# Performance work log

Measured on AMD Instinct MI355X. Metric: run time of the kernel, lower is better.

The kernel has to match this reference:

```python
import jax, jax.numpy as jnp
import numpy as np

NUM_JOINT_LIST = [8, 10, 12, 14, 16, 18, 20, 22, 24, 9, 13, 17]
NUM_GLOBAL_LIST = [1, 0, 1, 1, 0, 1, 1, 1, 0, 1, 1, 1]
M = len(NUM_JOINT_LIST)
B, T, JMAX = 16, 128, 24
H, HEADS, L, RANK = 256, 8, 4, 8
DH = H // HEADS
LAYERSCALE = 1e-4


def setup_inputs():
    key = jax.random.key(0)
    ks = jax.random.split(key, 40)
    m_idx = jax.random.randint(ks[0], (B,), 0, M)
    nj = jnp.array(NUM_JOINT_LIST)[m_idx]
    valid = jnp.arange(JMAX)[None, :] < nj[:, None]  # (B, J) real joints of each morphology
    jtype = jax.random.randint(ks[1], (B, JMAX), 0, 3)  # 0 slide, 1 hinge, 2 global
    has_g = (jnp.array(NUM_GLOBAL_LIST) > 0)[m_idx][:, None]
    jtype = jnp.where((jtype == 2) & ~has_g, 0, jtype)
    tile = lambda m: jnp.broadcast_to(m[:, None, :], (B, T, JMAX))
    slide_mask = tile((jtype == 0) & valid)
    hinge_mask = tile((jtype == 1) & valid)
    global_mask = tile((jtype == 2) & valid)
    act_mask = tile(valid)
    morph_mask = (valid[:, :, None] & valid[:, None, :]) | jnp.eye(JMAX, dtype=bool)[None]
    act = jax.random.normal(ks[2], (B, T, JMAX, 1), dtype=jnp.float32)
    s = 0.02
    inp = dict(act=act, slide_mask=slide_mask, hinge_mask=hinge_mask,
               global_mask=global_mask, act_mask=act_mask, morph_mask=morph_mask,
               m_idx=m_idx)
    inp['Ws'] = s * jax.random.normal(ks[3], (1, H)); inp['bs'] = jnp.zeros((H,))
    inp['Wh'] = s * jax.random.normal(ks[4], (1, H)); inp['bh'] = jnp.zeros((H,))
    inp['Wg'] = s * jax.random.normal(ks[5], (M, H))
    inp['Wact'] = s * jax.random.normal(ks[6], (1, H))
    pos = jax.random.normal(ks[7], (M, JMAX, H))
    pos_valid = jnp.arange(JMAX)[None, :, None] < jnp.array(NUM_JOINT_LIST)[:, None, None]
    inp['pos'] = pos * pos_valid  # rows beyond num_joint stay zero, as in the torch loop
    inp['ln1_s'] = jnp.ones((L, H)); inp['ln1_b'] = jnp.zeros((L, H))
    inp['Wqkv'] = s * jax.random.normal(ks[8], (L, H, 3 * H)); inp['bqkv'] = jnp.zeros((L, 3 * H))
    inp['loraA'] = s * jax.random.normal(ks[9], (L, M, H, RANK))
    inp['loraB'] = s * jax.random.normal(ks[10], (L, M, RANK, 3 * H))
    inp['Wo'] = s * jax.random.normal(ks[11], (L, H, H)); inp['bo'] = jnp.zeros((L, H))
    inp['ln2_s'] = jnp.ones((L, H)); inp['ln2_b'] = jnp.zeros((L, H))
    inp['W1'] = s * jax.random.normal(ks[12], (L, H, 4 * H)); inp['b1'] = jnp.zeros((L, 4 * H))
    inp['W2'] = s * jax.random.normal(ks[13], (L, 4 * H, H)); inp['b2'] = jnp.zeros((L, H))
    inp['g1'] = LAYERSCALE * jnp.ones((L, H)); inp['g2'] = LAYERSCALE * jnp.ones((L, H))
    inp['lnf_s'] = jnp.ones((H,)); inp['lnf_b'] = jnp.zeros((H,))
    return inp


def _ln(z, sc, bi):
    mu = z.mean(-1, keepdims=True)
    v = ((z - mu) ** 2).mean(-1, keepdims=True)
    return (z - mu) * jax.lax.rsqrt(v + 1e-5) * sc + bi


def reference(act, slide_mask, hinge_mask, global_mask, act_mask, morph_mask, m_idx,
              Ws, bs, Wh, bh, Wg, Wact, pos,
              ln1_s, ln1_b, Wqkv, bqkv, loraA, loraB, Wo, bo,
              ln2_s, ln2_b, W1, b1, W2, b2, g1, g2, lnf_s, lnf_b):
    has_g = (jnp.array(NUM_GLOBAL_LIST) > 0)[m_idx]  # (B,)
    a1 = act[..., :1]  # slide_dim = hinge_dim = num_global = 1
    emb = jnp.where(slide_mask[..., None], a1 @ Ws + bs, jnp.zeros((), act.dtype))
    emb = jnp.where(hinge_mask[..., None], a1 @ Wh + bh, emb)
    emb_g = a1 * Wg[m_idx][:, None, None, :]  # per-sample morphology-routed projection
    emb = jnp.where((global_mask & has_g[:, None, None])[..., None], emb_g, emb)
    y = emb + act_mask[..., None].astype(emb.dtype) * Wact[0]
    y = y + pos[m_idx][:, None]  # (B, T, J, H)
    Bv, Tv, J, _ = y.shape
    N = Bv * Tv
    x = y.reshape(N, J, H)
    amask = jnp.broadcast_to(morph_mask[:, None], (Bv, Tv, J, J)).reshape(N, J, J)
    t_idx = jnp.repeat(m_idx, Tv)  # (N,)
    neg = jnp.finfo(x.dtype).min
    scale = 1.0 / np.sqrt(DH)

    def block(x, lp):
        l1s, l1b, wqkv, bq, lA, lB, wo, bo_, l2s, l2b, w1, b1_, w2, b2_, gg1, gg2 = lp
        h = _ln(x, l1s, l1b)
        qkv = h @ wqkv + bq
        # per-task LoRA on qkv, gathered by morphology index
        qkv = qkv + jnp.einsum('njr,nrk->njk', jnp.einsum('njd,ndr->njr', h, lA[t_idx]), lB[t_idx])
        q, k, v = jnp.split(qkv, 3, axis=-1)
        q = q.reshape(N, J, HEADS, DH).transpose(0, 2, 1, 3)
        k = k.reshape(N, J, HEADS, DH).transpose(0, 2, 1, 3)
        v = v.reshape(N, J, HEADS, DH).transpose(0, 2, 1, 3)
        scores = jnp.einsum('nhid,nhjd->nhij', q, k) * scale
        scores = jnp.where(amask[:, None], scores, neg)
        attn = jax.nn.softmax(scores, axis=-1)
        o = jnp.einsum('nhij,nhjd->nhid', attn, v).transpose(0, 2, 1, 3).reshape(N, J, H)
        x = x + gg1 * (o @ wo + bo_)
        h2 = _ln(x, l2s, l2b)
        x = x + gg2 * (jax.nn.gelu(h2 @ w1 + b1_) @ w2 + b2_)
        return x, None

    x, _ = jax.lax.scan(block, x, (ln1_s, ln1_b, Wqkv, bqkv, loraA, loraB, Wo, bo,
                                   ln2_s, ln2_b, W1, b1, W2, b2, g1, g2))
    x = _ln(x, lnf_s, lnf_b)
    return x.reshape(Bv, Tv, J, H)
```

## Files before the change

### kernel.cpp

```cpp
#include <hip/hip_runtime.h>
#include <cstdint>
#include <cstddef>

#define B_     16
#define T_     128
#define J_     24
#define H_     256
#define HEADS_ 8
#define DH_    32
#define L_     4
#define RANK_  8
#define M_     12
#define NTOK   (B_*T_)
#define ROWS   (NTOK*J_)
#define HAS_G_MASK 3821

typedef __attribute__((ext_vector_type(8))) short short8;
typedef __attribute__((ext_vector_type(4))) float f32x4;

__constant__ int cNJ[M_] = {8, 10, 12, 14, 16, 18, 20, 22, 24, 9, 13, 17};

__device__ __forceinline__ float bf2f(unsigned short u) {
    union { unsigned int i; float f; } c; c.i = ((unsigned int)u) << 16; return c.f;
}
__device__ __forceinline__ unsigned short f2bf(float f) {
    union { float f; unsigned int i; } c; c.f = f;
    unsigned int x = c.i;
    return (unsigned short)((x + 0x7fffu + ((x >> 16) & 1u)) >> 16);
}
__device__ __forceinline__ void gload16(const void* g, void* l) {
    __builtin_amdgcn_global_load_lds((const __attribute__((address_space(1))) void*)g,
                                     (__attribute__((address_space(3))) void*)l, 16, 0, 0);
}

__global__ void zero_flag(int* f) { *f = 0; }

__global__ __launch_bounds__(256) void detect_kernel(
    const unsigned char* __restrict__ sl, const unsigned char* __restrict__ hi,
    const unsigned char* __restrict__ gl, const int* __restrict__ m_idx,
    int* __restrict__ flag) {
    int rj = blockIdx.x * 256 + threadIdx.x;
    if (rj >= ROWS) return;
    int b = rj / (T_ * J_);
    int j = rj % J_;
    int valid = (j < cNJ[m_idx[b]]) ? 1 : 0;
    int cnt = (sl[rj] != 0) + (hi[rj] != 0) + (gl[rj] != 0);
    if (cnt != valid) atomicOr(flag, 1);
}

__global__ void wconv_t(const float* __restrict__ W, unsigned short* __restrict__ WT,
                        int K, int Nc, int total) {
    int i = blockIdx.x * 256 + threadIdx.x;
    if (i >= total) return;
    int kn = K * Nc;
    int l = i / kn;
    int r = i - l * kn;
    int k = r / Nc;
    int n = r - k * Nc;
    WT[(size_t)l * kn + (size_t)n * K + k] = f2bf(W[i]);
}

__global__ __launch_bounds__(256) void embed_kernel(
    const float* __restrict__ act, const void* __restrict__ slide,
    const void* __restrict__ hinge, const void* __restrict__ glob,
    const int* __restrict__ m_idx, const int* __restrict__ flag,
    const float* __restrict__ Ws, const float* __restrict__ bs,
    const float* __restrict__ Wh, const float* __restrict__ bh,
    const float* __restrict__ Wg, const float* __restrict__ Wact,
    const float* __restrict__ pos, float* __restrict__ X) {
    int rj = (blockIdx.x << 2) + (threadIdx.x >> 6);
    int lane = threadIdx.x & 63;
    int b = rj / (T_ * J_);
    int j = rj % J_;
    int m = m_idx[b];
    bool valid = j < cNJ[m];
    bool s, hh, gl;
    if (*flag) {
        s  = ((const int*)slide)[rj] != 0;
        hh = ((const int*)hinge)[rj] != 0;
        gl = ((const int*)glob)[rj]  != 0;
    } else {
        s  = ((const unsigned char*)slide)[rj] != 0;
        hh = ((const unsigned char*)hinge)[rj] != 0;
        gl = ((const unsigned char*)glob)[rj]  != 0;
    }
    float a1 = act[rj];
    int h0 = lane << 2;
    float e0 = 0.f, e1 = 0.f, e2 = 0.f, e3 = 0.f;
    if (s) {
        float4 w = *(const float4*)(Ws + h0); float4 bb = *(const float4*)(bs + h0);
        e0 = a1 * w.x + bb.x; e1 = a1 * w.y + bb.y; e2 = a1 * w.z + bb.z; e3 = a1 * w.w + bb.w;
    } else if (hh) {
        float4 w = *(const float4*)(Wh + h0); float4 bb = *(const float4*)(bh + h0);
        e0 = a1 * w.x + bb.x; e1 = a1 * w.y + bb.y; e2 = a1 * w.z + bb.z; e3 = a1 * w.w + bb.w;
    } else if (gl && ((HAS_G_MASK >> m) & 1)) {
        float4 w = *(const float4*)(Wg + m * H_ + h0);
        e0 = a1 * w.x; e1 = a1 * w.y; e2 = a1 * w.z; e3 = a1 * w.w;
    }
    if (valid) {
        float4 wa = *(const float4*)(Wact + h0);
        e0 += wa.x; e1 += wa.y; e2 += wa.z; e3 += wa.w;
    }
    float4 pv = *(const float4*)(pos + (size_t)(m * J_ + j) * H_ + h0);
    float4 out; out.x = e0 + pv.x; out.y = e1 + pv.y; out.z = e2 + pv.z; out.w = e3 + pv.w;
    *(float4*)(X + ((size_t)rj << 8) + h0) = out;
}

template<bool LORA>
__global__ __launch_bounds__(256) void ln_kernel(
    const float* __restrict__ X, const float* __restrict__ sc, const float* __restrict__ bi,
    const float* __restrict__ lA, const int* __restrict__ m_idx,
    unsigned short* __restrict__ Hbf, float* __restrict__ Rbuf) {
    int row = (blockIdx.x << 2) + (threadIdx.x >> 6);
    int lane = threadIdx.x & 63;
    int h0 = lane << 2;
    float4 xv = *(const float4*)(X + ((size_t)row << 8) + h0);
    float s1 = xv.x + xv.y + xv.z + xv.w;
    float s2 = xv.x * xv.x + xv.y * xv.y + xv.z * xv.z + xv.w * xv.w;
    #pragma unroll
    for (int o = 32; o; o >>= 1) { s1 += __shfl_xor(s1, o); s2 += __shfl_xor(s2, o); }
    float mu = s1 * (1.f / H_);
    float var = s2 * (1.f / H_) - mu * mu;
    float rs = rsqrtf(var + 1e-5f);
    float4 scv = *(const float4*)(sc + h0);
    float4 biv = *(const float4*)(bi + h0);
    float hn0 = (xv.x - mu) * rs * scv.x + biv.x;
    float hn1 = (xv.y - mu) * rs * scv.y + biv.y;
    float hn2 = (xv.z - mu) * rs * scv.z + biv.z;
    float hn3 = (xv.w - mu) * rs * scv.w + biv.w;
    ushort4 o4; o4.x = f2bf(hn0); o4.y = f2bf(hn1); o4.z = f2bf(hn2); o4.w = f2bf(hn3);
    *(ushort4*)(Hbf + ((size_t)row << 8) + h0) = o4;
    if (LORA) {
        int t = m_idx[row / (J_ * T_)];
        const float* Ap = lA + (size_t)t * (H_ * RANK_) + h0 * RANK_;
        float4 av[8];
        #pragma unroll
        for (int c = 0; c < 8; ++c) av[c] = ((const float4*)Ap)[c];
        float hn[4] = {hn0, hn1, hn2, hn3};
        float p[RANK_];
        #pragma unroll
        for (int k = 0; k < RANK_; ++k) p[k] = 0.f;
        #pragma unroll
        for (int i = 0; i < 4; ++i)
            #pragma unroll
            for (int k = 0; k < RANK_; ++k) {
                int idx = i * RANK_ + k;
                float a = (idx & 3) == 0 ? av[idx >> 2].x : (idx & 3) == 1 ? av[idx >> 2].y
                        : (idx & 3) == 2 ? av[idx >> 2].z : av[idx >> 2].w;
                p[k] += hn[i] * a;
            }
        #pragma unroll
        for (int k = 0; k < RANK_; ++k)
            #pragma unroll
            for (int o = 32; o; o >>= 1) p[k] += __shfl_xor(p[k], o);
        if (lane == 0) {
            #pragma unroll
            for (int k = 0; k < RANK_; ++k) Rbuf[(size_t)row * RANK_ + k] = p[k];
        }
    }
}

__global__ __launch_bounds__(256) void lnf_kernel(
    float* __restrict__ X, const float* __restrict__ sc, const float* __restrict__ bi) {
    int row = (blockIdx.x << 2) + (threadIdx.x >> 6);
    int lane = threadIdx.x & 63;
    int h0 = lane << 2;
    float4 xv = *(const float4*)(X + ((size_t)row << 8) + h0);
    float s1 = xv.x + xv.y + xv.z + xv.w;
    float s2 = xv.x * xv.x + xv.y * xv.y + xv.z * xv.z + xv.w * xv.w;
    #pragma unroll
    for (int o = 32; o; o >>= 1) { s1 += __shfl_xor(s1, o); s2 += __shfl_xor(s2, o); }
    float mu = s1 * (1.f / H_);
    float var = s2 * (1.f / H_) - mu * mu;
    float rs = rsqrtf(var + 1e-5f);
    float4 scv = *(const float4*)(sc + h0);
    float4 biv = *(const float4*)(bi + h0);
    float4 out;
    out.x = (xv.x - mu) * rs * scv.x + biv.x;
    out.y = (xv.y - mu) * rs * scv.y + biv.y;
    out.z = (xv.z - mu) * rs * scv.z + biv.z;
    out.w = (xv.w - mu) * rs * scv.w + biv.w;
    *(float4*)(X + ((size_t)row << 8) + h0) = out;
}

template<int EPI>
__global__ __launch_bounds__(256) void gemm_k(
    const unsigned short* __restrict__ A, const unsigned short* __restrict__ BT,
    const float* __restrict__ bias,
    const float* __restrict__ aux1,
    const float* __restrict__ aux2,
    const int* __restrict__ m_idx,
    unsigned short* __restrict__ outB, float* __restrict__ outF,
    int K, int Nc) {
    __shared__ __align__(16) unsigned short As[128 * 64];
    __shared__ __align__(16) unsigned short Bs[128 * 64];
    int gx = gridDim.x;
    int nwg = gx * gridDim.y;
    int id = blockIdx.y * gx + blockIdx.x;
    int bx = blockIdx.x, by = blockIdx.y;
    if ((nwg & 7) == 0) {
        int q8 = nwg >> 3;
        int sid = (id & 7) * q8 + (id >> 3);
        bx = sid % gx; by = sid / gx;
    }
    int col0 = bx * 128;
    int row0 = by * 128;
    int tid = threadIdx.x;
    int wv = tid >> 6, lane = tid & 63;
    int wm = wv >> 1, wn = wv & 1;

    f32x4 acc[4][4];
    const f32x4 z = {0.f, 0.f, 0.f, 0.f};
    #pragma unroll
    for (int mi = 0; mi < 4; ++mi)
        #pragma unroll
        for (int ni = 0; ni < 4; ++ni) acc[mi][ni] = z;

    for (int k0 = 0; k0 < K; k0 += 64) {
        #pragma unroll
        for (int it = 0; it < 4; ++it) {
            int f = (tid << 4) + (it << 12);
            int r = f >> 7;
            int ce = (f & 127) >> 1;
            gload16(A  + (size_t)(row0 + r) * K + k0 + ce, (char*)As + f);
            gload16(BT + (size_t)(col0 + r) * K + k0 + ce, (char*)Bs + f);
        }
        __syncthreads();
        #pragma unroll
        for (int kk = 0; kk < 64; kk += 32) {
            short8 af[4], bfr[4];
            int ko = kk + ((lane >> 4) << 3);
            #pragma unroll
            for (int q = 0; q < 4; ++q) {
                af[q]  = *(const short8*)(As + ((wm * 64 + q * 16 + (lane & 15)) << 6) + ko);
                bfr[q] = *(const short8*)(Bs + ((wn * 64 + q * 16 + (lane & 15)) << 6) + ko);
            }
            #pragma unroll
            for (int mi = 0; mi < 4; ++mi)
                #pragma unroll
                for (int ni = 0; ni < 4; ++ni)
                    acc[mi][ni] = __builtin_amdgcn_mfma_f32_16x16x32_bf16(af[mi], bfr[ni], acc[mi][ni], 0, 0, 0);
        }
        __syncthreads();
    }

    int rbase = row0 + wm * 64 + ((lane >> 4) << 2);
    int cbase = col0 + wn * 64 + (lane & 15);

    if (EPI == 0) {
        int t = m_idx[row0 / (J_ * T_)];
        const float* lB = aux2 + (size_t)t * (RANK_ * 3 * H_);
        float lbv[4][RANK_];
        #pragma unroll
        for (int ni = 0; ni < 4; ++ni)
            #pragma unroll
            for (int kq = 0; kq < RANK_; ++kq)
                lbv[ni][kq] = lB[kq * (3 * H_) + cbase + ni * 16];
        #pragma unroll
        for (int mi = 0; mi < 4; ++mi) {
            #pragma unroll
            for (int r = 0; r < 4; ++r) {
                int row = rbase + mi * 16 + r;
                const float* Rr = aux1 + (size_t)row * RANK_;
                float rv[RANK_];
                #pragma unroll
                for (int kq = 0; kq < RANK_; ++kq) rv[kq] = Rr[kq];
                #pragma unroll
                for (int ni = 0; ni < 4; ++ni) {
                    int col = cbase + ni * 16;
                    float val = acc[mi][ni][r] + bias[col];
                    #pragma unroll
                    for (int kq = 0; kq < RANK_; ++kq) val += rv[kq] * lbv[ni][kq];
                    outB[(size_t)row * (3 * H_) + col] = f2bf(val);
                }
            }
        }
    } else if (EPI == 1) {
        #pragma unroll
        for (int mi = 0; mi < 4; ++mi)
            #pragma unroll
            for (int r = 0; r < 4; ++r) {
                int row = rbase + mi * 16 + r;
                #pragma unroll
                for (int ni = 0; ni < 4; ++ni) {
                    int col = cbase + ni * 16;
                    float u = acc[mi][ni][r] + bias[col];
                    float zz = 0.7978845608028654f * (u + 0.044715f * u * u * u);
                    float tt = __expf(-2.f * fabsf(zz));
                    float th = (1.f - tt) / (1.f + tt);
                    th = zz < 0.f ? -th : th;
                    outB[(size_t)row * Nc + col] = f2bf(0.5f * u * (1.f + th));
                }
            }
    } else {
        #pragma unroll
        for (int mi = 0; mi < 4; ++mi)
            #pragma unroll
            for (int r = 0; r < 4; ++r) {
                int row = rbase + mi * 16 + r;
                #pragma unroll
                for (int ni = 0; ni < 4; ++ni) {
                    int col = cbase + ni * 16;
                    float u = acc[mi][ni][r] + bias[col];
                    outF[(size_t)row * H_ + col] += aux1[col] * u;
                }
            }
    }
}

__global__ __launch_bounds__(64) void attn_kernel(
    const unsigned short* __restrict__ QKV, const int* __restrict__ m_idx,
    unsigned short* __restrict__ O) {
    int blk = blockIdx.x;
    int n = blk >> 3;
    int hd = blk & 7;
    int b = n >> 7;
    int lane = threadIdx.x;
    int nj = cNJ[m_idx[b]];
    __shared__ float q[J_][DH_], k[J_][DH_], v[J_][DH_], sc[J_][J_];

    const unsigned short* base = QKV + (size_t)n * J_ * (3 * H_) + hd * DH_;
    #pragma unroll
    for (int it = 0; it < 3; ++it) {
        int idx = it * 256 + (lane << 2);
        int j = idx >> 5, d = idx & 31;
        const unsigned short* p = base + j * (3 * H_) + d;
        ushort4 qv = *(const ushort4*)(p);
        ushort4 kv = *(const ushort4*)(p + H_);
        ushort4 vv = *(const ushort4*)(p + 2 * H_);
        q[j][d] = bf2f(qv.x); q[j][d+1] = bf2f(qv.y); q[j][d+2] = bf2f(qv.z); q[j][d+3] = bf2f(qv.w);
        k[j][d] = bf2f(kv.x); k[j][d+1] = bf2f(kv.y); k[j][d+2] = bf2f(kv.z); k[j][d+3] = bf2f(kv.w);
        v[j][d] = bf2f(vv.x); v[j][d+1] = bf2f(vv.y); v[j][d+2] = bf2f(vv.z); v[j][d+3] = bf2f(vv.w);
    }
    __syncthreads();

    const float scale = 0.17677669529663687f;
    #pragma unroll
    for (int it = 0; it < 9; ++it) {
        int idx = it * 64 + lane;
        int i = idx / J_, j = idx - i * J_;
        float s = 0.f;
        #pragma unroll
        for (int d = 0; d < DH_; ++d) s += q[i][d] * k[j][d];
        bool ok = (i < nj && j < nj) || (i == j);
        sc[i][j] = ok ? s * scale : -3.4028234663852886e38f;
    }
    __syncthreads();

    if (lane < J_) {
        float mx = -3.4028234663852886e38f;
        #pragma unroll
        for (int j = 0; j < J_; ++j) mx = fmaxf(mx, sc[lane][j]);
        float sm = 0.f;
        #pragma unroll
        for (int j = 0; j < J_; ++j) { float e = __expf(sc[lane][j] - mx); sc[lane][j] = e; sm += e; }
        float inv = 1.f / sm;
        #pragma unroll
        for (int j = 0; j < J_; ++j) sc[lane][j] *= inv;
    }
    __syncthreads();

    #pragma unroll
    for (int it = 0; it < 6; ++it) {
        int idx = it * 128 + (lane << 1);
        int i = idx >> 5, d = idx & 31;
        float o0 = 0.f, o1 = 0.f;
        #pragma unroll
        for (int j = 0; j < J_; ++j) {
            float a = sc[i][j];
            o0 += a * v[j][d];
            o1 += a * v[j][d + 1];
        }
        ushort2 st; st.x = f2bf(o0); st.y = f2bf(o1);
        *(ushort2*)(O + (size_t)(n * J_ + i) * H_ + hd * DH_ + d) = st;
    }
}

extern "C" void kernel_launch(void* const* d_in, const int* in_sizes, int n_in,
                              void* d_out, int out_size, void* d_ws, size_t ws_size,
                              hipStream_t stream) {
    (void)in_sizes; (void)n_in; (void)out_size; (void)ws_size;
    const float* act   = (const float*)d_in[0];
    const void*  slide = d_in[1];
    const void*  hinge = d_in[2];
    const void*  glob  = d_in[3];
    const int* m_idx  = (const int*)d_in[6];
    const float* Ws   = (const float*)d_in[7];
    const float* bs   = (const float*)d_in[8];
    const float* Wh   = (const float*)d_in[9];
    const float* bh   = (const float*)d_in[10];
    const float* Wg   = (const float*)d_in[11];
    const float* Wact = (const float*)d_in[12];
    const float* pos  = (const float*)d_in[13];
    const float* ln1s = (const float*)d_in[14];
    const float* ln1b = (const float*)d_in[15];
    const float* Wqkv = (const float*)d_in[16];
    const float* bqkv = (const float*)d_in[17];
    const float* loraA= (const float*)d_in[18];
    const float* loraB= (const float*)d_in[19];
    const float* Wo   = (const float*)d_in[20];
    const float* bo   = (const float*)d_in[21];
    const float* ln2s = (const float*)d_in[22];
    const float* ln2b = (const float*)d_in[23];
    const float* W1   = (const float*)d_in[24];
    const float* b1   = (const float*)d_in[25];
    const float* W2   = (const float*)d_in[26];
    const float* b2   = (const float*)d_in[27];
    const float* g1   = (const float*)d_in[28];
    const float* g2   = (const float*)d_in[29];
    const float* lnfs = (const float*)d_in[30];
    const float* lnfb = (const float*)d_in[31];

    float* X = (float*)d_out;

    size_t off = 0;
    char* ws = (char*)d_ws;
    auto nxt = [&](size_t bytes) -> char* {
        char* p = ws + off; off += (bytes + 255) & ~(size_t)255; return p;
    };
    int*            dflag = (int*)nxt(256);
    unsigned short* Hbf   = (unsigned short*)nxt((size_t)ROWS * H_ * 2);
    unsigned short* QKVG  = (unsigned short*)nxt((size_t)ROWS * 1024 * 2);
    float*          Rbuf  = (float*)nxt((size_t)ROWS * RANK_ * 4);
    unsigned short* WqkvT = (unsigned short*)nxt((size_t)L_ * H_ * 768 * 2);
    unsigned short* WoT   = (unsigned short*)nxt((size_t)L_ * H_ * H_ * 2);
    unsigned short* W1T   = (unsigned short*)nxt((size_t)L_ * H_ * 1024 * 2);
    unsigned short* W2T   = (unsigned short*)nxt((size_t)L_ * 1024 * H_ * 2);
    unsigned short* Obf   = Hbf;

    zero_flag<<<1, 1, 0, stream>>>(dflag);
    detect_kernel<<<(ROWS + 255) / 256, 256, 0, stream>>>(
        (const unsigned char*)slide, (const unsigned char*)hinge,
        (const unsigned char*)glob, m_idx, dflag);

    wconv_t<<<(L_ * H_ * 768 + 255) / 256, 256, 0, stream>>>(Wqkv, WqkvT, H_, 768, L_ * H_ * 768);
    wconv_t<<<(L_ * H_ * H_  + 255) / 256, 256, 0, stream>>>(Wo,   WoT,   H_, H_,  L_ * H_ * H_);
    wconv_t<<<(L_ * H_ * 1024+ 255) / 256, 256, 0, stream>>>(W1,   W1T,   H_, 1024,L_ * H_ * 1024);
    wconv_t<<<(L_ * 1024* H_ + 255) / 256, 256, 0, stream>>>(W2,   W2T,   1024, H_,L_ * 1024 * H_);

    embed_kernel<<<ROWS / 4, 256, 0, stream>>>(act, slide, hinge, glob, m_idx, dflag,
                                               Ws, bs, Wh, bh, Wg, Wact, pos, X);

    for (int l = 0; l < L_; ++l) {
        ln_kernel<true><<<ROWS / 4, 256, 0, stream>>>(X, ln1s + l * H_, ln1b + l * H_,
                                                      loraA + (size_t)l * M_ * H_ * RANK_, m_idx, Hbf, Rbuf);
        gemm_k<0><<<dim3(6, 384), 256, 0, stream>>>(Hbf, WqkvT + (size_t)l * H_ * 768,
                                                    bqkv + l * 768, Rbuf,
                                                    loraB + (size_t)l * M_ * RANK_ * 768, m_idx,
                                                    QKVG, nullptr, H_, 768);
        attn_kernel<<<NTOK * HEADS_, 64, 0, stream>>>(QKVG, m_idx, Obf);
        gemm_k<2><<<dim3(2, 384), 256, 0, stream>>>(Obf, WoT + (size_t)l * H_ * H_,
                                                    bo + l * H_, g1 + l * H_, nullptr, nullptr,
                                                    nullptr, X, H_, H_);
        ln_kernel<false><<<ROWS / 4, 256, 0, stream>>>(X, ln2s + l * H_, ln2b + l * H_,
                                                       nullptr, nullptr, Hbf, nullptr);
        gemm_k<1><<<dim3(8, 384), 256, 0, stream>>>(Hbf, W1T + (size_t)l * H_ * 1024,
                                                    b1 + l * 1024, nullptr, nullptr, nullptr,
                                                    QKVG, nullptr, H_, 1024);
        gemm_k<2><<<dim3(2, 384), 256, 0, stream>>>(QKVG, W2T + (size_t)l * 1024 * H_,
                                                    b2 + l * H_, g2 + l * H_, nullptr, nullptr,
                                                    nullptr, X, 1024, H_);
    }

    lnf_kernel<<<ROWS / 4, 256, 0, stream>>>(X, lnfs, lnfb);
}
```

Before: 1.623 ms.

## Restructure attention kernel: four heads per block, packed bf16 LDS, register softmax

The attention kernel now runs four heads per 256-thread block, one wavefront per head, and drops all block barriers. Q, K and V stay as packed bf16 pairs in padded shared memory, with K stored transposed, instead of being expanded to fp32. Each row's scores are computed by two lanes and the softmax runs in registers, with cross-lane shuffles for the max and the sum. The aim is to cut LDS traffic, bank conflicts, barrier stalls and the serial 24-lane softmax. The risk is that it relies on wavefront-lockstep ordering of LDS writes and reads without a barrier, and on higher register pressure.

```diff
diff --git a/kernel.cpp b/kernel.cpp
--- a/kernel.cpp
+++ b/kernel.cpp
@@ -27,6 +27,9 @@
     union { float f; unsigned int i; } c; c.f = f;
     unsigned int x = c.i;
     return (unsigned short)((x + 0x7fffu + ((x >> 16) & 1u)) >> 16);
+}
+__device__ __forceinline__ float asf(unsigned int u) {
+    union { unsigned int i; float f; } c; c.i = u; return c.f;
 }
 __device__ __forceinline__ void gload16(const void* g, void* l) {
     __builtin_amdgcn_global_load_lds((const __attribute__((address_space(1))) void*)g,
@@ -308,71 +311,99 @@
     }
 }
 
-__global__ __launch_bounds__(64) void attn_kernel(
+__global__ __launch_bounds__(256) void attn_kernel(
     const unsigned short* __restrict__ QKV, const int* __restrict__ m_idx,
     unsigned short* __restrict__ O) {
-    int blk = blockIdx.x;
-    int n = blk >> 3;
-    int hd = blk & 7;
-    int b = n >> 7;
-    int lane = threadIdx.x;
-    int nj = cNJ[m_idx[b]];
-    __shared__ float q[J_][DH_], k[J_][DH_], v[J_][DH_], sc[J_][J_];
-
-    const unsigned short* base = QKV + (size_t)n * J_ * (3 * H_) + hd * DH_;
+    __shared__ unsigned int q2s[4][24][18];
+    __shared__ unsigned int k2s[4][16][26];
+    __shared__ unsigned int v2s[4][24][18];
+    __shared__ float       scs[4][24][27];
+    int w = threadIdx.x >> 6, lane = threadIdx.x & 63;
+    int n = blockIdx.x >> 1;
+    int hd = ((blockIdx.x & 1) << 2) + w;
+    int nj = cNJ[m_idx[n >> 7]];
+    unsigned int (*q2)[18] = q2s[w];
+    unsigned int (*k2)[26] = k2s[w];
+    unsigned int (*v2)[18] = v2s[w];
+    float (*sc)[27] = scs[w];
+
+    const unsigned short* base = QKV + (size_t)n * (J_ * 768) + hd * DH_;
+
     #pragma unroll
     for (int it = 0; it < 3; ++it) {
-        int idx = it * 256 + (lane << 2);
-        int j = idx >> 5, d = idx & 31;
-        const unsigned short* p = base + j * (3 * H_) + d;
-        ushort4 qv = *(const ushort4*)(p);
-        ushort4 kv = *(const ushort4*)(p + H_);
-        ushort4 vv = *(const ushort4*)(p + 2 * H_);
-        q[j][d] = bf2f(qv.x); q[j][d+1] = bf2f(qv.y); q[j][d+2] = bf2f(qv.z); q[j][d+3] = bf2f(qv.w);
-        k[j][d] = bf2f(kv.x); k[j][d+1] = bf2f(kv.y); k[j][d+2] = bf2f(kv.z); k[j][d+3] = bf2f(kv.w);
-        v[j][d] = bf2f(vv.x); v[j][d+1] = bf2f(vv.y); v[j][d+2] = bf2f(vv.z); v[j][d+3] = bf2f(vv.w);
-    }
-    __syncthreads();
-
-    const float scale = 0.17677669529663687f;
-    #pragma unroll
-    for (int it = 0; it < 9; ++it) {
-        int idx = it * 64 + lane;
-        int i = idx / J_, j = idx - i * J_;
-        float s = 0.f;
-        #pragma unroll
-        for (int d = 0; d < DH_; ++d) s += q[i][d] * k[j][d];
-        bool ok = (i < nj && j < nj) || (i == j);
-        sc[i][j] = ok ? s * scale : -3.4028234663852886e38f;
-    }
-    __syncthreads();
-
-    if (lane < J_) {
-        float mx = -3.4028234663852886e38f;
-        #pragma unroll
-        for (int j = 0; j < J_; ++j) mx = fmaxf(mx, sc[lane][j]);
+        int r = it * 64 + lane;
+        int j = r >> 3, d0 = (r & 7) << 2, d2 = d0 >> 1;
+        ushort4 x = *(const ushort4*)(base + (size_t)j * 768 + d0);
+        q2[j][d2]     = (unsigned int)x.x | ((unsigned int)x.y << 16);
+        q2[j][d2 + 1] = (unsigned int)x.z | ((unsigned int)x.w << 16);
+    }
+    #pragma unroll
+    for (int it = 0; it < 3; ++it) {
+        int r = it * 64 + lane;
+        int j = r >> 3, d0 = (r & 7) << 2, d2 = d0 >> 1;
+        ushort4 x = *(const ushort4*)(base + (size_t)j * 768 + 256 + d0);
+        k2[d2][j]     = (unsigned int)x.x | ((unsigned int)x.y << 16);
+        k2[d2 + 1][j] = (unsigned int)x.z | ((unsigned int)x.w << 16);
+    }
+    #pragma unroll
+    for (int it = 0; it < 3; ++it) {
+        int r = it * 64 + lane;
+        int j = r >> 3, d0 = (r & 7) << 2, d2 = d0 >> 1;
+        ushort4 x = *(const ushort4*)(base + (size_t)j * 768 + 512 + d0);
+        v2[j][d2]     = (unsigned int)x.x | ((unsigned int)x.y << 16);
+        v2[j][d2 + 1] = (unsigned int)x.z | ((unsigned int)x.w << 16);
+    }
+
+    int i = lane >> 1, half = lane & 1;
+    if (lane < 48) {
+        float qf[32];
+        #pragma unroll
+        for (int d2 = 0; d2 < 16; ++d2) {
+            unsigned int x = q2[i][d2];
+            qf[2 * d2]     = asf(x << 16);
+            qf[2 * d2 + 1] = asf(x & 0xffff0000u);
+        }
+        int jb = half * 12;
+        float s[12];
+        #pragma unroll
+        for (int jj = 0; jj < 12; ++jj) {
+            int j = jb + jj;
+            float acc = 0.f;
+            #pragma unroll
+            for (int d2 = 0; d2 < 16; ++d2) {
+                unsigned int x = k2[d2][j];
+                acc += qf[2 * d2] * asf(x << 16);
+                acc += qf[2 * d2 + 1] * asf(x & 0xffff0000u);
+            }
+            bool ok = (i < nj && j < nj) || (i == j);
+            s[jj] = ok ? acc * 0.17677669529663687f : -1e30f;
+        }
+        float mx = s[0];
+        #pragma unroll
+        for (int jj = 1; jj < 12; ++jj) mx = fmaxf(mx, s[jj]);
+        mx = fmaxf(mx, __shfl_xor(mx, 1));
         float sm = 0.f;
         #pragma unroll
-        for (int j = 0; j < J_; ++j) { float e = __expf(sc[lane][j] - mx); sc[lane][j] = e; sm += e; }
+        for (int jj = 0; jj < 12; ++jj) { float e = __expf(s[jj] - mx); s[jj] = e; sm += e; }
+        sm += __shfl_xor(sm, 1);
         float inv = 1.f / sm;
         #pragma unroll
-        for (int j = 0; j < J_; ++j) sc[lane][j] *= inv;
-    }
-    __syncthreads();
+        for (int jj = 0; jj < 12; ++jj) sc[i][jb + jj] = s[jj] * inv;
+    }
 
     #pragma unroll
     for (int it = 0; it < 6; ++it) {
-        int idx = it * 128 + (lane << 1);
-        int i = idx >> 5, d = idx & 31;
-        float o0 = 0.f, o1 = 0.f;
+        int i2 = it * 4 + (lane >> 4), d2 = lane & 15;
+        float olo = 0.f, ohi = 0.f;
         #pragma unroll
         for (int j = 0; j < J_; ++j) {
-            float a = sc[i][j];
-            o0 += a * v[j][d];
-            o1 += a * v[j][d + 1];
-        }
-        ushort2 st; st.x = f2bf(o0); st.y = f2bf(o1);
-        *(ushort2*)(O + (size_t)(n * J_ + i) * H_ + hd * DH_ + d) = st;
+            float p = sc[i2][j];
+            unsigned int x = v2[j][d2];
+            olo += p * asf(x << 16);
+            ohi += p * asf(x & 0xffff0000u);
+        }
+        unsigned int o = (unsigned int)f2bf(olo) | ((unsigned int)f2bf(ohi) << 16);
+        *(unsigned int*)(O + (size_t)(n * J_ + i2) * H_ + hd * DH_ + 2 * d2) = o;
     }
 }
 
@@ -448,7 +479,7 @@
                                                     bqkv + l * 768, Rbuf,
                                                     loraB + (size_t)l * M_ * RANK_ * 768, m_idx,
                                                     QKVG, nullptr, H_, 768);
-        attn_kernel<<<NTOK * HEADS_, 64, 0, stream>>>(QKVG, m_idx, Obf);
+        attn_kernel<<<NTOK * 2, 256, 0, stream>>>(QKVG, m_idx, Obf);
         gemm_k<2><<<dim3(2, 384), 256, 0, stream>>>(Obf, WoT + (size_t)l * H_ * H_,
                                                     bo + l * H_, g1 + l * H_, nullptr, nullptr,
                                                     nullptr, X, H_, H_);
```

Result: faster. 1.445 ms (-11.0%).
